# Kernel tuning notes

Measured on AMD Instinct MI355X. Metric: run time of the kernel, lower is better.

The kernel has to match this reference:

```python
import math
import jax, jax.numpy as jnp
import numpy as np

BATCH, L, H, M, K = 16, 4096, 256, 256, 4

def setup_inputs() -> dict:
    key = jax.random.key(0)
    ks = jax.random.split(key, 12)
    inputs = jax.random.normal(ks[0], (BATCH, L, H), jnp.float32)
    b_std = 1.0 / math.sqrt(H)
    c_std = 1.0 / math.sqrt(M)
    B_param = jax.random.uniform(ks[1], (M, H, 2), jnp.float32, -b_std, b_std)
    C_param = jax.random.uniform(ks[2], (H, M, 2), jnp.float32, -c_std, c_std)
    D = jax.random.normal(ks[3], (H,), jnp.float32)
    enc_w = jax.random.normal(ks[4], (H, H), jnp.float32) * (1.0 / math.sqrt(H))
    enc_b = jnp.zeros((H,), jnp.float32)
    conv_w = jax.random.normal(ks[5], (H, 1, K), jnp.float32) * (1.0 / math.sqrt(K))
    conv_b = jnp.zeros((H,), jnp.float32)
    # ring init: r in [0.9,1.0], theta in (0,pi)
    r0 = jnp.sqrt(jax.random.uniform(ks[6], (M,), jnp.float32) * (1.0 - 0.81) + 0.81)
    r0 = jnp.clip(r0, 0.9, 0.999)
    th0 = jax.random.uniform(ks[7], (M,), jnp.float32, 0.05, math.pi - 0.05)
    r_logit_base = jnp.log(r0 / (1.0 - r0))
    th_atanh_base = jnp.arctanh(th0 / math.pi)
    # heads are zero-init in the module; use small random so the selective path is exercised
    r_head_w = jax.random.normal(ks[8], (M, H), jnp.float32) * 0.01
    th_head_w = jax.random.normal(ks[9], (M, H), jnp.float32) * 0.01
    dt_base = jax.random.normal(ks[10], (M,), jnp.float32) * 0.5
    inj_head_w = jax.random.normal(ks[11], (M, H), jnp.float32) * 0.01
    return {"inputs": inputs, "B_param": B_param, "C_param": C_param, "D": D,
            "enc_w": enc_w, "enc_b": enc_b, "conv_w": conv_w, "conv_b": conv_b,
            "r_logit_base": r_logit_base, "th_atanh_base": th_atanh_base,
            "r_head_w": r_head_w, "th_head_w": th_head_w, "dt_base": dt_base,
            "inj_head_w": inj_head_w}

def _forward(inputs, B_param, C_param, D, enc_w, enc_b, conv_w, conv_b,
             r_logit_base, th_atanh_base, r_head_w, th_head_w, dt_base, inj_head_w):
    silu = jax.nn.silu
    # encoder: linear -> SiLU -> depthwise causal conv (left pad K-1) -> SiLU
    feats = silu(inputs @ enc_w.T + enc_b)                      # (B,L,H)
    fc = jnp.transpose(feats, (0, 2, 1))                        # (B,H,L)
    conv = jax.lax.conv_general_dilated(
        fc, conv_w, window_strides=(1,), padding=[(K - 1, 0)],
        dimension_numbers=("NCH", "OIH", "NCH"), feature_group_count=H)
    feats = silu(jnp.transpose(conv + conv_b[None, :, None], (0, 2, 1)))  # (B,L,H)
    # spectral conditioning
    r = jax.nn.sigmoid(r_logit_base + feats @ r_head_w.T)       # (B,L,M)
    theta = math.pi * jnp.tanh(th_atanh_base + feats @ th_head_w.T)
    dt = jax.nn.sigmoid(dt_base)                                # (M,) per_step_dt=False
    dtc = jnp.maximum(dt, 1e-6)
    r2 = jnp.maximum(r * r, 1e-8)
    A = jnp.maximum((r2 - 2.0 * r * jnp.cos(theta) + 1.0) / (dtc * dtc * r2), 0.0)
    G = jnp.maximum((1.0 - r2) / (dtc * r2), 0.0)
    # complex input projection + selective injection gate
    bu = jax.lax.complex(inputs @ B_param[..., 0].T, inputs @ B_param[..., 1].T)  # (B,L,M) c64
    gate = jax.nn.sigmoid(feats @ inj_head_w.T)
    bu = bu * gate
    # time-major for scan
    A_s = jnp.transpose(A, (1, 0, 2))
    G_s = jnp.transpose(G, (1, 0, 2))
    bu_s = jnp.transpose(bu, (1, 0, 2))
    z0 = jnp.zeros((inputs.shape[0], M), jnp.complex64)
    x0 = jnp.zeros((inputs.shape[0], M), jnp.complex64)

    def step(carry, t_in):  # imex1 variant
        z, x = carry
        A_t, G_t, bu_t = t_in
        S = 1.0 + dtc * G_t
        z = (z + dtc * (-A_t * x + bu_t)) / jnp.maximum(S, 1e-6)
        x = x + dtc * z
        return (z, x), x

    _, xs = jax.lax.scan(step, (z0, x0), (A_s, G_s, bu_s))      # (L,B,M) complex64
    proj = (jnp.einsum("lbm,hm->lbh", xs.real, C_param[..., 0])
            - jnp.einsum("lbm,hm->lbh", xs.imag, C_param[..., 1]))
    proj = jnp.transpose(proj, (1, 0, 2))                       # (B,L,H)
    return proj + D * inputs

def reference(inputs, B_param, C_param, D, enc_w, enc_b, conv_w, conv_b,
              r_logit_base, th_atanh_base, r_head_w, th_head_w, dt_base, inj_head_w):
    return _forward(inputs, B_param, C_param, D, enc_w, enc_b, conv_w, conv_b,
                    r_logit_base, th_atanh_base, r_head_w, th_head_w, dt_base, inj_head_w)
```

## Files before the change

### kernel.cpp

```cpp
#include <hip/hip_runtime.h>

#define H_ 256
#define M_ 256
#define L_ 4096
#define B_ 16
#define PI_F 3.14159265358979323846f

typedef unsigned short u16;
typedef __attribute__((ext_vector_type(8))) short short8v;
typedef __attribute__((ext_vector_type(4))) float floatx4;
typedef __attribute__((ext_vector_type(2))) float floatx2;

__device__ __forceinline__ float sigm(float x) { return 1.0f / (1.0f + expf(-x)); }
__device__ __forceinline__ u16 f2bf(float f) {
    unsigned int u = __float_as_uint(f);
    unsigned int r = (u + 0x7fff + ((u >> 16) & 1)) >> 16;
    return (u16)r;
}
__device__ __forceinline__ float bf2f(u16 h) { return __uint_as_float(((unsigned int)h) << 16); }
__device__ __forceinline__ void split2(float x, u16& h, u16& l) {
    h = f2bf(x);
    l = f2bf(x - bf2f(h));
}

__global__ __launch_bounds__(256) void k_prep(const float* __restrict__ Bp,
                                              const float* __restrict__ Cp,
                                              const float* __restrict__ enc_w,
                                              const float* __restrict__ Wr,
                                              const float* __restrict__ Wt,
                                              const float* __restrict__ Wg,
                                              const float* __restrict__ dtb,
                                              u16* __restrict__ EWhi, u16* __restrict__ EWlo,
                                              u16* __restrict__ HWhi, u16* __restrict__ HWlo,
                                              u16* __restrict__ GWhi,
                                              u16* __restrict__ WBh,
                                              u16* __restrict__ Chath,
                                              float* __restrict__ dtc, float* __restrict__ idt,
                                              float* __restrict__ idt2) {
    int tid = blockIdx.x * 256 + threadIdx.x;
    if (tid < M_) {
        float d = fmaxf(sigm(dtb[tid]), 1e-6f);
        dtc[tid] = d;
        idt[tid] = 1.0f / d;
        idt2[tid] = 1.0f / (d * d);
    }
    u16 h, l;
    split2(enc_w[tid], h, l); EWhi[tid] = h; EWlo[tid] = l;
    split2(Wr[tid], h, l);    HWhi[tid] = h; HWlo[tid] = l;
    split2(Wt[tid], h, l);    HWhi[65536 + tid] = h; HWlo[65536 + tid] = l;
    GWhi[tid] = f2bf(Wg[tid]);
    WBh[tid]         = f2bf(Bp[2 * tid + 0]);
    WBh[65536 + tid] = f2bf(Bp[2 * tid + 1]);
    int hh = tid >> 8, m = tid & (M_ - 1);
    Chath[hh * 512 + 2 * m + 0] = f2bf(Cp[2 * tid + 0]);
    Chath[hh * 512 + 2 * m + 1] = f2bf(-Cp[2 * tid + 1]);
}

__global__ __launch_bounds__(256) void k_zero(float* __restrict__ p, int n) {
    int i = blockIdx.x * 256 + threadIdx.x;
    if (i < n) p[i] = 0.0f;
}

template <int NH, int NPROD, int EPI, bool AGLOB>
__global__ __launch_bounds__(256) void k_sgemm(const float* __restrict__ A,
                                               const u16* __restrict__ Whi,
                                               const u16* __restrict__ Wlo,
                                               void* __restrict__ OUTv,
                                               const u16* __restrict__ g16,
                                               const float* __restrict__ p0,
                                               const float* __restrict__ p1,
                                               const float* __restrict__ p2,
                                               const float* __restrict__ p3,
                                               int K, int C, int t0) {
    constexpr int LOR = (NPROD == 3) ? 128 : 1;
    constexpr int NBL = (NPROD == 3) ? NH : 1;
    __shared__ u16 Ah[128][40];
    __shared__ u16 Al[LOR][40];
    __shared__ u16 Bh[NH][128][40];
    __shared__ u16 Bl[NBL][LOR][40];
    const int tid = threadIdx.x;
    const int tpb = C >> 7;
    const int batch = blockIdx.y / tpb;
    const int i0 = (blockIdx.y % tpb) << 7;
    const int colBase = blockIdx.x << 7;
    const int aRow0 = AGLOB ? (batch * L_ + t0 + i0) : (batch * C + i0);
    const int oRow0 = batch * C + i0;
    const int arow = tid >> 1, aseg = (tid & 1) << 4;
    const float* pa = &A[(size_t)(aRow0 + arow) * K + aseg];
    float4 ra0 = *(const float4*)pa, ra1 = *(const float4*)(pa + 4);
    float4 ra2 = *(const float4*)(pa + 8), ra3 = *(const float4*)(pa + 12);
    const int lane = tid & 63, wv = tid >> 6;
    const int wr = wv >> 1, wc = wv & 1;
    const int fr = lane & 15, kg = lane >> 4;
    floatx4 acc[NH][4][4];
#pragma unroll
    for (int h = 0; h < NH; ++h)
#pragma unroll
        for (int i = 0; i < 4; ++i)
#pragma unroll
            for (int j = 0; j < 4; ++j) acc[h][i][j] = (floatx4){0.f, 0.f, 0.f, 0.f};
    const int KT = K >> 5;
    for (int kt = 0; kt < KT; ++kt) {
        short8v rbh[NH][2], rbl[NBL][2];
#pragma unroll
        for (int h = 0; h < NH; ++h) {
            const u16* pb = &Whi[(size_t)h * 65536 + (size_t)(colBase + arow) * K + kt * 32 + aseg];
            rbh[h][0] = *(const short8v*)pb; rbh[h][1] = *(const short8v*)(pb + 8);
            if (NPROD == 3) {
                const u16* pl = &Wlo[(size_t)h * 65536 + (size_t)(colBase + arow) * K + kt * 32 + aseg];
                rbl[h][0] = *(const short8v*)pl; rbl[h][1] = *(const short8v*)(pl + 8);
            }
        }
        __syncthreads();
        {
            u16 hb[16], lb[16];
            float v[16] = {ra0.x, ra0.y, ra0.z, ra0.w, ra1.x, ra1.y, ra1.z, ra1.w,
                           ra2.x, ra2.y, ra2.z, ra2.w, ra3.x, ra3.y, ra3.z, ra3.w};
#pragma unroll
            for (int s = 0; s < 16; ++s) {
                if (NPROD == 3) split2(v[s], hb[s], lb[s]);
                else hb[s] = f2bf(v[s]);
            }
            *(short8v*)&Ah[arow][aseg] = *(short8v*)&hb[0];
            *(short8v*)&Ah[arow][aseg + 8] = *(short8v*)&hb[8];
            if (NPROD == 3) {
                *(short8v*)&Al[arow][aseg] = *(short8v*)&lb[0];
                *(short8v*)&Al[arow][aseg + 8] = *(short8v*)&lb[8];
            }
        }
#pragma unroll
        for (int h = 0; h < NH; ++h) {
            *(short8v*)&Bh[h][arow][aseg] = rbh[h][0];
            *(short8v*)&Bh[h][arow][aseg + 8] = rbh[h][1];
            if (NPROD == 3) {
                *(short8v*)&Bl[h][arow][aseg] = rbl[h][0];
                *(short8v*)&Bl[h][arow][aseg + 8] = rbl[h][1];
            }
        }
        __syncthreads();
        if (kt + 1 < KT) {
            pa += 32;
            ra0 = *(const float4*)pa; ra1 = *(const float4*)(pa + 4);
            ra2 = *(const float4*)(pa + 8); ra3 = *(const float4*)(pa + 12);
        }
        short8v afh[4], afl[4];
#pragma unroll
        for (int i = 0; i < 4; ++i) afh[i] = *(short8v*)&Ah[wr * 64 + i * 16 + fr][kg << 3];
        if (NPROD == 3) {
#pragma unroll
            for (int i = 0; i < 4; ++i) afl[i] = *(short8v*)&Al[wr * 64 + i * 16 + fr][kg << 3];
        }
#pragma unroll
        for (int h = 0; h < NH; ++h) {
            short8v bfh[4], bfl[4];
#pragma unroll
            for (int j = 0; j < 4; ++j) bfh[j] = *(short8v*)&Bh[h][wc * 64 + j * 16 + fr][kg << 3];
            if (h < NBL && NPROD == 3) {
#pragma unroll
                for (int j = 0; j < 4; ++j) bfl[j] = *(short8v*)&Bl[h][wc * 64 + j * 16 + fr][kg << 3];
            }
#pragma unroll
            for (int i = 0; i < 4; ++i)
#pragma unroll
                for (int j = 0; j < 4; ++j) {
                    floatx4 t = acc[h][i][j];
                    if (NPROD == 3) {
                        t = __builtin_amdgcn_mfma_f32_16x16x32_bf16(afl[i], bfh[j], t, 0, 0, 0);
                        t = __builtin_amdgcn_mfma_f32_16x16x32_bf16(afh[i], bfl[j], t, 0, 0, 0);
                    }
                    t = __builtin_amdgcn_mfma_f32_16x16x32_bf16(afh[i], bfh[j], t, 0, 0, 0);
                    acc[h][i][j] = t;
                }
        }
    }
#pragma unroll
    for (int i = 0; i < 4; ++i)
#pragma unroll
        for (int j = 0; j < 4; ++j) {
            int rbase = wr * 64 + i * 16 + (kg << 2);
            int col = colBase + wc * 64 + j * 16 + fr;
#pragma unroll
            for (int r = 0; r < 4; ++r) {
                int orow = oRow0 + rbase + r;
                if (EPI == 1) {
                    float v = acc[0][i][j][r] + p0[col];
                    ((float*)OUTv)[(size_t)orow * 256 + col] = v * sigm(v);
                } else if (EPI == 2) {
                    ((u16*)OUTv)[(size_t)orow * 256 + col] = f2bf(sigm(acc[0][i][j][r]));
                } else if (EPI == 0) {
                    float rr = sigm(p0[col] + acc[0][i][j][r]);
                    float th = PI_F * tanhf(p1[col] + acc[1][i][j][r]);
                    float r2 = fmaxf(rr * rr, 1e-8f);
                    float Av = fmaxf((r2 - 2.0f * rr * cosf(th) + 1.0f) * p3[col] / r2, 0.0f);
                    float Gv = fmaxf((1.0f - r2) * p2[col] / r2, 0.0f);
                    floatx2 o = (floatx2){Av, Gv};
                    __builtin_nontemporal_store(o, (floatx2*)&((float*)OUTv)[((size_t)orow * 256 + col) * 2]);
                } else {
                    float g = bf2f(g16[(size_t)orow * 256 + col]);
#pragma unroll
                    for (int h = 0; h < NH; ++h)
                        __builtin_nontemporal_store(f2bf(acc[h][i][j][r] * g),
                                                    &((u16*)OUTv)[(size_t)orow * 512 + h * 256 + col]);
                }
            }
        }
}

__global__ __launch_bounds__(256) void k_conv(const float* __restrict__ F0,
                                              const float* __restrict__ TAIL,
                                              const float* __restrict__ cw,
                                              const float* __restrict__ cb,
                                              float* __restrict__ F,
                                              int t0, int C) {
    int idx = blockIdx.x * 256 + threadIdx.x;
    int h = idx & (H_ - 1);
    int rl = idx >> 8;
    int b = rl / C;
    int dtl = rl - b * C;
    int t = t0 + dtl;
    float w0 = cw[h * 4 + 0], w1 = cw[h * 4 + 1], w2 = cw[h * 4 + 2], w3 = cw[h * 4 + 3];
    float acc = cb[h];
    acc = fmaf(F0[(size_t)rl * H_ + h], w3, acc);
#pragma unroll
    for (int kk = 1; kk <= 3; ++kk) {
        float w = (kk == 1) ? w2 : (kk == 2) ? w1 : w0;
        if (t - kk >= 0) {
            float src;
            if (dtl - kk >= 0) src = F0[(size_t)(rl - kk) * H_ + h];
            else               src = TAIL[((b * 3 + (3 + dtl - kk)) << 8) + h];
            acc = fmaf(src, w, acc);
        }
    }
    F[(size_t)rl * H_ + h] = acc * sigm(acc);
}

__global__ __launch_bounds__(256) void k_tail(const float* __restrict__ F0,
                                              float* __restrict__ TAIL, int C) {
    int b = blockIdx.x / 3, j = blockIdx.x % 3, h = threadIdx.x;
    TAIL[((b * 3 + j) << 8) + h] = F0[((size_t)(b * C + C - 3 + j) << 8) + h];
}

#define SEG_ 64
__global__ __launch_bounds__(256) void k_scan1(const float* __restrict__ AGf2,
                                               const u16* __restrict__ BUh,
                                               const float* __restrict__ dtc_,
                                               float* __restrict__ SEGM,
                                               float* __restrict__ SEGV,
                                               int C) {
    int m = threadIdx.x;
    int nseg = C >> 6;
    int b = blockIdx.x / nseg;
    int s = blockIdx.x - b * nseg;
    float dt = dtc_[m];
    size_t row0 = (size_t)b * C + s * SEG_;
    float a = 1.f, bb = 0.f, c = 0.f, d = 1.f;
    float vzr = 0.f, vzi = 0.f, vxr = 0.f, vxi = 0.f;
    for (int t = 0; t < SEG_; ++t) {
        size_t row = row0 + t;
        float2 ag = *(const float2*)&AGf2[(row * 256 + m) * 2];
        float br = bf2f(BUh[row * 512 + m]);
        float bi = bf2f(BUh[row * 512 + 256 + m]);
        float S = fmaf(dt, ag.y, 1.0f);
        float e = 1.0f / fmaxf(S, 1e-6f);
        float sa = e;
        float sb = -dt * ag.x * e;
        float sc = dt * e;
        float sd = fmaf(dt, sb, 1.0f);
        float na = fmaf(sa, a, sb * c), nb = fmaf(sa, bb, sb * d);
        float nc = fmaf(sc, a, sd * c), nd = fmaf(sc, bb, sd * d);
        float wz = dt * e;
        float nvzr = fmaf(sa, vzr, fmaf(sb, vxr, wz * br));
        float nvzi = fmaf(sa, vzi, fmaf(sb, vxi, wz * bi));
        float nvxr = fmaf(sc, vzr, fmaf(sd, vxr, dt * wz * br));
        float nvxi = fmaf(sc, vzi, fmaf(sd, vxi, dt * wz * bi));
        a = na; bb = nb; c = nc; d = nd;
        vzr = nvzr; vzi = nvzi; vxr = nvxr; vxi = nvxi;
    }
    size_t o = ((size_t)blockIdx.x * M_ + m) * 4;
    *(float4*)&SEGM[o] = make_float4(a, bb, c, d);
    *(float4*)&SEGV[o] = make_float4(vzr, vzi, vxr, vxi);
}

__global__ __launch_bounds__(256) void k_scan2(const float* __restrict__ SEGM,
                                               const float* __restrict__ SEGV,
                                               float* __restrict__ carry,
                                               float* __restrict__ PRE,
                                               int C) {
    int m = threadIdx.x;
    int b = blockIdx.x;
    int nseg = C >> 6;
    float4 st = *(float4*)&carry[(size_t)(b * M_ + m) * 4];
    for (int s = 0; s < nseg; ++s) {
        size_t o = ((size_t)(b * nseg + s) * M_ + m) * 4;
        *(float4*)&PRE[o] = st;
        float4 Mm = *(const float4*)&SEGM[o];
        float4 Vv = *(const float4*)&SEGV[o];
        float nzr = fmaf(Mm.x, st.x, fmaf(Mm.y, st.z, Vv.x));
        float nzi = fmaf(Mm.x, st.y, fmaf(Mm.y, st.w, Vv.y));
        float nxr = fmaf(Mm.z, st.x, fmaf(Mm.w, st.z, Vv.z));
        float nxi = fmaf(Mm.z, st.y, fmaf(Mm.w, st.w, Vv.w));
        st = make_float4(nzr, nzi, nxr, nxi);
    }
    *(float4*)&carry[(size_t)(b * M_ + m) * 4] = st;
}

__global__ __launch_bounds__(256) void k_scan3p(const float* __restrict__ AGf2,
                                                const u16* __restrict__ BUh,
                                                const float* __restrict__ dtc_,
                                                const float* __restrict__ PRE,
                                                const u16* __restrict__ Chath,
                                                const float* __restrict__ Dv,
                                                const float* __restrict__ X0,
                                                float* __restrict__ OUT,
                                                int t0, int C) {
    __shared__ u16 XT[32][520];
    __shared__ u16 Bs[256][40];
    const int tid = threadIdx.x;
    const int m = tid;
    const int nseg = C >> 6;
    const int b = blockIdx.x / nseg;
    const int s = blockIdx.x - b * nseg;
    const float dt = dtc_[m];
    float4 st = *(const float4*)&PRE[((size_t)blockIdx.x * M_ + m) * 4];
    float zr = st.x, zi = st.y, xr = st.z, xi = st.w;
    const size_t row0 = (size_t)b * C + s * SEG_;
    const int grow0 = b * L_ + t0 + s * SEG_;
    const int lane = tid & 63, wc = tid >> 6;
    const int fr = lane & 15, kg = lane >> 4;
#pragma unroll
    for (int half = 0; half < 2; ++half) {
        for (int t = 0; t < 32; ++t) {
            size_t row = row0 + half * 32 + t;
            floatx2 ag = __builtin_nontemporal_load((const floatx2*)&AGf2[(row * 256 + m) * 2]);
            float br = bf2f(__builtin_nontemporal_load(&BUh[row * 512 + m]));
            float bi = bf2f(__builtin_nontemporal_load(&BUh[row * 512 + 256 + m]));
            float S = fmaf(dt, ag[1], 1.0f);
            float inv = 1.0f / fmaxf(S, 1e-6f);
            zr = fmaf(dt, fmaf(-ag[0], xr, br), zr) * inv;
            zi = fmaf(dt, fmaf(-ag[0], xi, bi), zi) * inv;
            xr = fmaf(dt, zr, xr);
            xi = fmaf(dt, zi, xi);
            unsigned int pk = (unsigned int)f2bf(xr) | ((unsigned int)f2bf(xi) << 16);
            *(unsigned int*)&XT[t][2 * m] = pk;
        }
        __syncthreads();
        floatx4 pacc[2][4];
#pragma unroll
        for (int i = 0; i < 2; ++i)
#pragma unroll
            for (int j = 0; j < 4; ++j) pacc[i][j] = (floatx4){0.f, 0.f, 0.f, 0.f};
        for (int kc = 0; kc < 16; ++kc) {
            const u16* pc = &Chath[(size_t)tid * 512 + kc * 32];
            short8v c0 = *(const short8v*)pc;
            short8v c1 = *(const short8v*)(pc + 8);
            short8v c2 = *(const short8v*)(pc + 16);
            short8v c3 = *(const short8v*)(pc + 24);
            *(short8v*)&Bs[tid][0]  = c0;
            *(short8v*)&Bs[tid][8]  = c1;
            *(short8v*)&Bs[tid][16] = c2;
            *(short8v*)&Bs[tid][24] = c3;
            __syncthreads();
            short8v af[2], bf[4];
#pragma unroll
            for (int i = 0; i < 2; ++i) af[i] = *(short8v*)&XT[i * 16 + fr][kc * 32 + (kg << 3)];
#pragma unroll
            for (int j = 0; j < 4; ++j) bf[j] = *(short8v*)&Bs[wc * 64 + j * 16 + fr][kg << 3];
#pragma unroll
            for (int i = 0; i < 2; ++i)
#pragma unroll
                for (int j = 0; j < 4; ++j)
                    pacc[i][j] = __builtin_amdgcn_mfma_f32_16x16x32_bf16(af[i], bf[j], pacc[i][j], 0, 0, 0);
            __syncthreads();
        }
#pragma unroll
        for (int i = 0; i < 2; ++i)
#pragma unroll
            for (int j = 0; j < 4; ++j) {
                int col = wc * 64 + j * 16 + fr;
#pragma unroll
                for (int r = 0; r < 4; ++r) {
                    int grow = grow0 + half * 32 + i * 16 + (kg << 2) + r;
                    float x0 = __builtin_nontemporal_load(&X0[(size_t)grow * 256 + col]);
                    __builtin_nontemporal_store(fmaf(Dv[col], x0, pacc[i][j][r]),
                                                &OUT[(size_t)grow * 256 + col]);
                }
            }
        __syncthreads();
    }
}

extern "C" void kernel_launch(void* const* d_in, const int* in_sizes, int n_in,
                              void* d_out, int out_size, void* d_ws, size_t ws_size,
                              hipStream_t stream) {
    const float* inputs = (const float*)d_in[0];
    const float* Bp     = (const float*)d_in[1];
    const float* Cp     = (const float*)d_in[2];
    const float* Dv     = (const float*)d_in[3];
    const float* enc_w  = (const float*)d_in[4];
    const float* enc_b  = (const float*)d_in[5];
    const float* conv_w = (const float*)d_in[6];
    const float* conv_b = (const float*)d_in[7];
    const float* rlb    = (const float*)d_in[8];
    const float* tab    = (const float*)d_in[9];
    const float* Wr     = (const float*)d_in[10];
    const float* Wt     = (const float*)d_in[11];
    const float* dtb    = (const float*)d_in[12];
    const float* Wg     = (const float*)d_in[13];

    int C = 4096;
    while (C > 128) {
        size_t need = (size_t)B_ * C * 5632 + (48ull << 20);
        if (need <= ws_size) break;
        C >>= 1;
    }

    char* ws = (char*)d_ws;
    size_t off = 0;
    auto alloc = [&](size_t bytes) -> char* {
        char* p = ws + off;
        off = (off + bytes + 1023) & ~(size_t)1023;
        return p;
    };
    const int rows = B_ * C;
    const int nseg = C >> 6;
    float* F0   = (float*)alloc((size_t)rows * 256 * 4);
    float* F    = (float*)alloc((size_t)rows * 256 * 4);
    float* AGf2 = (float*)alloc((size_t)rows * 512 * 4);
    u16*   GTh  = (u16*)alloc((size_t)rows * 256 * 2);
    u16*   BUh  = (u16*)alloc((size_t)rows * 512 * 2);
    float* SEGM = (float*)alloc((size_t)B_ * nseg * M_ * 16);
    float* SEGV = (float*)alloc((size_t)B_ * nseg * M_ * 16);
    float* PRE  = (float*)alloc((size_t)B_ * nseg * M_ * 16);
    u16* EWhi = (u16*)alloc(65536 * 2);
    u16* EWlo = (u16*)alloc(65536 * 2);
    u16* HWhi = (u16*)alloc(2 * 65536 * 2);
    u16* HWlo = (u16*)alloc(2 * 65536 * 2);
    u16* GWhi = (u16*)alloc(65536 * 2);
    u16* WBh  = (u16*)alloc(2 * 65536 * 2);
    u16* Chath= (u16*)alloc(2 * 65536 * 2);
    float* dtc  = (float*)alloc(1024);
    float* idt  = (float*)alloc(1024);
    float* idt2 = (float*)alloc(1024);
    float* carry= (float*)alloc(B_ * M_ * 16);
    float* TAIL = (float*)alloc(B_ * 3 * 256 * 4);

    const int NC = L_ / C;
    const int tpb = C >> 7;

    k_prep<<<256, 256, 0, stream>>>(Bp, Cp, enc_w, Wr, Wt, Wg, dtb,
                                    EWhi, EWlo, HWhi, HWlo, GWhi, WBh, Chath, dtc, idt, idt2);
    k_zero<<<(B_ * M_ * 4 + 255) / 256, 256, 0, stream>>>(carry, B_ * M_ * 4);

    for (int c = 0; c < NC; ++c) {
        int t0 = c * C;
        k_sgemm<1, 3, 1, true><<<dim3(2, B_ * tpb), 256, 0, stream>>>(
            inputs, EWhi, EWlo, F0, nullptr, enc_b, nullptr, nullptr, nullptr, 256, C, t0);
        k_conv<<<rows, 256, 0, stream>>>(F0, TAIL, conv_w, conv_b, F, t0, C);
        if (NC > 1) k_tail<<<B_ * 3, 256, 0, stream>>>(F0, TAIL, C);
        k_sgemm<2, 3, 0, false><<<dim3(2, B_ * tpb), 256, 0, stream>>>(
            F, HWhi, HWlo, AGf2, nullptr, rlb, tab, idt, idt2, 256, C, t0);
        k_sgemm<1, 1, 2, false><<<dim3(2, B_ * tpb), 256, 0, stream>>>(
            F, GWhi, nullptr, GTh, nullptr, nullptr, nullptr, nullptr, nullptr, 256, C, t0);
        k_sgemm<2, 1, 3, true><<<dim3(2, B_ * tpb), 256, 0, stream>>>(
            inputs, WBh, nullptr, BUh, GTh, nullptr, nullptr, nullptr, nullptr, 256, C, t0);
        k_scan1<<<B_ * nseg, 256, 0, stream>>>(AGf2, BUh, dtc, SEGM, SEGV, C);
        k_scan2<<<B_, 256, 0, stream>>>(SEGM, SEGV, carry, PRE, C);
        k_scan3p<<<B_ * nseg, 256, 0, stream>>>(AGf2, BUh, dtc, PRE, Chath, Dv, inputs,
                                                (float*)d_out, t0, C);
    }
}
```

Baseline: 728.2 us.

## Load weight MFMA fragments directly from global memory, dropping LDS staging

Both the split-bf16 GEMM kernel and the scan projection kernel stop copying weight tiles (Whi/Wlo and Chath) into shared memory. Each wave now reads its MFMA B fragments straight from global memory. This removes the LDS stores and frees LDS for occupancy, and in the scan kernel it also drops two barriers per k-chunk. In exchange, each wave re-fetches the same weight rows from global/L2 with 16-byte strided accesses and loses the register prefetch that overlapped the weight load with compute.

```diff
diff --git a/kernel.cpp b/kernel.cpp
--- a/kernel.cpp
+++ b/kernel.cpp
@@ -73,11 +73,8 @@
                                                const float* __restrict__ p3,
                                                int K, int C, int t0) {
     constexpr int LOR = (NPROD == 3) ? 128 : 1;
-    constexpr int NBL = (NPROD == 3) ? NH : 1;
     __shared__ u16 Ah[128][40];
     __shared__ u16 Al[LOR][40];
-    __shared__ u16 Bh[NH][128][40];
-    __shared__ u16 Bl[NBL][LOR][40];
     const int tid = threadIdx.x;
     const int tpb = C >> 7;
     const int batch = blockIdx.y / tpb;
@@ -101,16 +98,6 @@
             for (int j = 0; j < 4; ++j) acc[h][i][j] = (floatx4){0.f, 0.f, 0.f, 0.f};
     const int KT = K >> 5;
     for (int kt = 0; kt < KT; ++kt) {
-        short8v rbh[NH][2], rbl[NBL][2];
-#pragma unroll
-        for (int h = 0; h < NH; ++h) {
-            const u16* pb = &Whi[(size_t)h * 65536 + (size_t)(colBase + arow) * K + kt * 32 + aseg];
-            rbh[h][0] = *(const short8v*)pb; rbh[h][1] = *(const short8v*)(pb + 8);
-            if (NPROD == 3) {
-                const u16* pl = &Wlo[(size_t)h * 65536 + (size_t)(colBase + arow) * K + kt * 32 + aseg];
-                rbl[h][0] = *(const short8v*)pl; rbl[h][1] = *(const short8v*)(pl + 8);
-            }
-        }
         __syncthreads();
         {
             u16 hb[16], lb[16];
@@ -128,15 +115,6 @@
                 *(short8v*)&Al[arow][aseg + 8] = *(short8v*)&lb[8];
             }
         }
-#pragma unroll
-        for (int h = 0; h < NH; ++h) {
-            *(short8v*)&Bh[h][arow][aseg] = rbh[h][0];
-            *(short8v*)&Bh[h][arow][aseg + 8] = rbh[h][1];
-            if (NPROD == 3) {
-                *(short8v*)&Bl[h][arow][aseg] = rbl[h][0];
-                *(short8v*)&Bl[h][arow][aseg + 8] = rbl[h][1];
-            }
-        }
         __syncthreads();
         if (kt + 1 < KT) {
             pa += 32;
@@ -154,10 +132,14 @@
         for (int h = 0; h < NH; ++h) {
             short8v bfh[4], bfl[4];
 #pragma unroll
-            for (int j = 0; j < 4; ++j) bfh[j] = *(short8v*)&Bh[h][wc * 64 + j * 16 + fr][kg << 3];
-            if (h < NBL && NPROD == 3) {
-#pragma unroll
-                for (int j = 0; j < 4; ++j) bfl[j] = *(short8v*)&Bl[h][wc * 64 + j * 16 + fr][kg << 3];
+            for (int j = 0; j < 4; ++j)
+                bfh[j] = *(const short8v*)&Whi[(size_t)h * 65536 +
+                          (size_t)(colBase + wc * 64 + j * 16 + fr) * K + kt * 32 + (kg << 3)];
+            if (NPROD == 3) {
+#pragma unroll
+                for (int j = 0; j < 4; ++j)
+                    bfl[j] = *(const short8v*)&Wlo[(size_t)h * 65536 +
+                              (size_t)(colBase + wc * 64 + j * 16 + fr) * K + kt * 32 + (kg << 3)];
             }
 #pragma unroll
             for (int i = 0; i < 4; ++i)
@@ -314,7 +296,6 @@
                                                 float* __restrict__ OUT,
                                                 int t0, int C) {
     __shared__ u16 XT[32][520];
-    __shared__ u16 Bs[256][40];
     const int tid = threadIdx.x;
     const int m = tid;
     const int nseg = C >> 6;
@@ -350,27 +331,17 @@
 #pragma unroll
             for (int j = 0; j < 4; ++j) pacc[i][j] = (floatx4){0.f, 0.f, 0.f, 0.f};
         for (int kc = 0; kc < 16; ++kc) {
-            const u16* pc = &Chath[(size_t)tid * 512 + kc * 32];
-            short8v c0 = *(const short8v*)pc;
-            short8v c1 = *(const short8v*)(pc + 8);
-            short8v c2 = *(const short8v*)(pc + 16);
-            short8v c3 = *(const short8v*)(pc + 24);
-            *(short8v*)&Bs[tid][0]  = c0;
-            *(short8v*)&Bs[tid][8]  = c1;
-            *(short8v*)&Bs[tid][16] = c2;
-            *(short8v*)&Bs[tid][24] = c3;
-            __syncthreads();
             short8v af[2], bf[4];
 #pragma unroll
             for (int i = 0; i < 2; ++i) af[i] = *(short8v*)&XT[i * 16 + fr][kc * 32 + (kg << 3)];
 #pragma unroll
-            for (int j = 0; j < 4; ++j) bf[j] = *(short8v*)&Bs[wc * 64 + j * 16 + fr][kg << 3];
+            for (int j = 0; j < 4; ++j)
+                bf[j] = *(const short8v*)&Chath[(size_t)(wc * 64 + j * 16 + fr) * 512 + kc * 32 + (kg << 3)];
 #pragma unroll
             for (int i = 0; i < 2; ++i)
 #pragma unroll
                 for (int j = 0; j < 4; ++j)
                     pacc[i][j] = __builtin_amdgcn_mfma_f32_16x16x32_bf16(af[i], bf[j], pacc[i][j], 0, 0, 0);
-            __syncthreads();
         }
 #pragma unroll
         for (int i = 0; i < 2; ++i)
```

Measured after the change: 840.5 us. +15.4%, slower.

## Pre-split GEMM inputs to bf16 planes and stage tiles via global_load_lds

Applied to the files above, without the earlier changes.

Converts the fp32 inputs and the conv output into bf16 hi/lo planes ahead of time, so the GEMM kernels no longer split fp32 to bf16 inside their main loop. The GEMM is rewritten to copy each tile straight from global memory into LDS with global_load_lds into unpadded planes, which removes the register round trip and the convert work. Costs include an extra conversion pass over the whole input, a larger workspace, possible LDS bank conflicts from the unpadded 32-wide rows, and a second barrier per k-step with no prefetch overlap.

```diff
diff --git a/kernel.cpp b/kernel.cpp
--- a/kernel.cpp
+++ b/kernel.cpp
@@ -21,6 +21,11 @@
 __device__ __forceinline__ void split2(float x, u16& h, u16& l) {
     h = f2bf(x);
     l = f2bf(x - bf2f(h));
+}
+__device__ __forceinline__ void gload16(const u16* gsrc, u16* ldst) {
+    typedef __attribute__((address_space(1))) const unsigned int GU;
+    typedef __attribute__((address_space(3))) unsigned int LU;
+    __builtin_amdgcn_global_load_lds((GU*)gsrc, (LU*)ldst, 16, 0, 0);
 }
 
 __global__ __launch_bounds__(256) void k_prep(const float* __restrict__ Bp,
@@ -61,8 +66,22 @@
     if (i < n) p[i] = 0.0f;
 }
 
-template <int NH, int NPROD, int EPI, bool AGLOB>
-__global__ __launch_bounds__(256) void k_sgemm(const float* __restrict__ A,
+__global__ __launch_bounds__(256) void k_tobf(const float* __restrict__ X,
+                                              u16* __restrict__ Xhi, u16* __restrict__ Xlo) {
+    size_t i = ((size_t)blockIdx.x * 256 + threadIdx.x) * 8;
+    float4 a = *(const float4*)&X[i];
+    float4 b = *(const float4*)&X[i + 4];
+    float v[8] = {a.x, a.y, a.z, a.w, b.x, b.y, b.z, b.w};
+    u16 hb[8], lb[8];
+#pragma unroll
+    for (int s = 0; s < 8; ++s) split2(v[s], hb[s], lb[s]);
+    *(short8v*)&Xhi[i] = *(short8v*)hb;
+    *(short8v*)&Xlo[i] = *(short8v*)lb;
+}
+
+template <int NH, int NSPLIT, int EPI, bool AGLOB>
+__global__ __launch_bounds__(256) void k_bgemm(const u16* __restrict__ Ahi,
+                                               const u16* __restrict__ Alo,
                                                const u16* __restrict__ Whi,
                                                const u16* __restrict__ Wlo,
                                                void* __restrict__ OUTv,
@@ -71,13 +90,10 @@
                                                const float* __restrict__ p1,
                                                const float* __restrict__ p2,
                                                const float* __restrict__ p3,
-                                               int K, int C, int t0) {
-    constexpr int LOR = (NPROD == 3) ? 128 : 1;
-    constexpr int NBL = (NPROD == 3) ? NH : 1;
-    __shared__ u16 Ah[128][40];
-    __shared__ u16 Al[LOR][40];
-    __shared__ u16 Bh[NH][128][40];
-    __shared__ u16 Bl[NBL][LOR][40];
+                                               int C, int t0) {
+    constexpr int NA = (NSPLIT > 0) ? 2 : 1;
+    constexpr int NPLANES = NA + NH + NSPLIT;
+    __shared__ u16 LDS[NPLANES * 4096];
     const int tid = threadIdx.x;
     const int tpb = C >> 7;
     const int batch = blockIdx.y / tpb;
@@ -85,13 +101,20 @@
     const int colBase = blockIdx.x << 7;
     const int aRow0 = AGLOB ? (batch * L_ + t0 + i0) : (batch * C + i0);
     const int oRow0 = batch * C + i0;
-    const int arow = tid >> 1, aseg = (tid & 1) << 4;
-    const float* pa = &A[(size_t)(aRow0 + arow) * K + aseg];
-    float4 ra0 = *(const float4*)pa, ra1 = *(const float4*)(pa + 4);
-    float4 ra2 = *(const float4*)(pa + 8), ra3 = *(const float4*)(pa + 12);
+    const u16* gp[NPLANES];
+    {
+        int idx = 0;
+        gp[idx++] = Ahi + (size_t)aRow0 * 256;
+        if (NA == 2) gp[idx++] = Alo + (size_t)aRow0 * 256;
+#pragma unroll
+        for (int h = 0; h < NH; ++h) gp[idx++] = Whi + (size_t)h * 65536 + (size_t)colBase * 256;
+#pragma unroll
+        for (int h = 0; h < NSPLIT; ++h) gp[idx++] = Wlo + (size_t)h * 65536 + (size_t)colBase * 256;
+    }
     const int lane = tid & 63, wv = tid >> 6;
     const int wr = wv >> 1, wc = wv & 1;
     const int fr = lane & 15, kg = lane >> 4;
+    const int wbase = (tid & 192) * 8;
     floatx4 acc[NH][4][4];
 #pragma unroll
     for (int h = 0; h < NH; ++h)
@@ -99,72 +122,50 @@
         for (int i = 0; i < 4; ++i)
 #pragma unroll
             for (int j = 0; j < 4; ++j) acc[h][i][j] = (floatx4){0.f, 0.f, 0.f, 0.f};
-    const int KT = K >> 5;
-    for (int kt = 0; kt < KT; ++kt) {
-        short8v rbh[NH][2], rbl[NBL][2];
-#pragma unroll
-        for (int h = 0; h < NH; ++h) {
-            const u16* pb = &Whi[(size_t)h * 65536 + (size_t)(colBase + arow) * K + kt * 32 + aseg];
-            rbh[h][0] = *(const short8v*)pb; rbh[h][1] = *(const short8v*)(pb + 8);
-            if (NPROD == 3) {
-                const u16* pl = &Wlo[(size_t)h * 65536 + (size_t)(colBase + arow) * K + kt * 32 + aseg];
-                rbl[h][0] = *(const short8v*)pl; rbl[h][1] = *(const short8v*)(pl + 8);
-            }
-        }
+    for (int kt = 0; kt < 8; ++kt) {
+#pragma unroll
+        for (int p = 0; p < NPLANES; ++p)
+#pragma unroll
+            for (int q = 0; q < 2; ++q) {
+                int slot = q * 256 + tid;
+                const u16* src = gp[p] + (size_t)(slot >> 2) * 256 + kt * 32 + (slot & 3) * 8;
+                gload16(src, &LDS[p * 4096 + q * 2048 + wbase]);
+            }
         __syncthreads();
-        {
-            u16 hb[16], lb[16];
-            float v[16] = {ra0.x, ra0.y, ra0.z, ra0.w, ra1.x, ra1.y, ra1.z, ra1.w,
-                           ra2.x, ra2.y, ra2.z, ra2.w, ra3.x, ra3.y, ra3.z, ra3.w};
-#pragma unroll
-            for (int s = 0; s < 16; ++s) {
-                if (NPROD == 3) split2(v[s], hb[s], lb[s]);
-                else hb[s] = f2bf(v[s]);
-            }
-            *(short8v*)&Ah[arow][aseg] = *(short8v*)&hb[0];
-            *(short8v*)&Ah[arow][aseg + 8] = *(short8v*)&hb[8];
-            if (NPROD == 3) {
-                *(short8v*)&Al[arow][aseg] = *(short8v*)&lb[0];
-                *(short8v*)&Al[arow][aseg + 8] = *(short8v*)&lb[8];
-            }
-        }
-#pragma unroll
-        for (int h = 0; h < NH; ++h) {
-            *(short8v*)&Bh[h][arow][aseg] = rbh[h][0];
-            *(short8v*)&Bh[h][arow][aseg + 8] = rbh[h][1];
-            if (NPROD == 3) {
-                *(short8v*)&Bl[h][arow][aseg] = rbl[h][0];
-                *(short8v*)&Bl[h][arow][aseg + 8] = rbl[h][1];
-            }
-        }
-        __syncthreads();
-        if (kt + 1 < KT) {
-            pa += 32;
-            ra0 = *(const float4*)pa; ra1 = *(const float4*)(pa + 4);
-            ra2 = *(const float4*)(pa + 8); ra3 = *(const float4*)(pa + 12);
-        }
         short8v afh[4], afl[4];
 #pragma unroll
-        for (int i = 0; i < 4; ++i) afh[i] = *(short8v*)&Ah[wr * 64 + i * 16 + fr][kg << 3];
-        if (NPROD == 3) {
-#pragma unroll
-            for (int i = 0; i < 4; ++i) afl[i] = *(short8v*)&Al[wr * 64 + i * 16 + fr][kg << 3];
+        for (int i = 0; i < 4; ++i) {
+            int row = wr * 64 + i * 16 + fr;
+            afh[i] = *(short8v*)&LDS[row * 32 + kg * 8];
+        }
+        if (NA == 2) {
+#pragma unroll
+            for (int i = 0; i < 4; ++i) {
+                int row = wr * 64 + i * 16 + fr;
+                afl[i] = *(short8v*)&LDS[4096 + row * 32 + kg * 8];
+            }
         }
 #pragma unroll
         for (int h = 0; h < NH; ++h) {
             short8v bfh[4], bfl[4];
 #pragma unroll
-            for (int j = 0; j < 4; ++j) bfh[j] = *(short8v*)&Bh[h][wc * 64 + j * 16 + fr][kg << 3];
-            if (h < NBL && NPROD == 3) {
-#pragma unroll
-                for (int j = 0; j < 4; ++j) bfl[j] = *(short8v*)&Bl[h][wc * 64 + j * 16 + fr][kg << 3];
+            for (int j = 0; j < 4; ++j) {
+                int row = wc * 64 + j * 16 + fr;
+                bfh[j] = *(short8v*)&LDS[(NA + h) * 4096 + row * 32 + kg * 8];
+            }
+            if (h < NSPLIT) {
+#pragma unroll
+                for (int j = 0; j < 4; ++j) {
+                    int row = wc * 64 + j * 16 + fr;
+                    bfl[j] = *(short8v*)&LDS[(NA + NH + h) * 4096 + row * 32 + kg * 8];
+                }
             }
 #pragma unroll
             for (int i = 0; i < 4; ++i)
 #pragma unroll
                 for (int j = 0; j < 4; ++j) {
                     floatx4 t = acc[h][i][j];
-                    if (NPROD == 3) {
+                    if (h < NSPLIT) {
                         t = __builtin_amdgcn_mfma_f32_16x16x32_bf16(afl[i], bfh[j], t, 0, 0, 0);
                         t = __builtin_amdgcn_mfma_f32_16x16x32_bf16(afh[i], bfl[j], t, 0, 0, 0);
                     }
@@ -172,6 +173,7 @@
                     acc[h][i][j] = t;
                 }
         }
+        __syncthreads();
     }
 #pragma unroll
     for (int i = 0; i < 4; ++i)
@@ -210,7 +212,8 @@
                                               const float* __restrict__ TAIL,
                                               const float* __restrict__ cw,
                                               const float* __restrict__ cb,
-                                              float* __restrict__ F,
+                                              u16* __restrict__ Fhi,
+                                              u16* __restrict__ Flo,
                                               int t0, int C) {
     int idx = blockIdx.x * 256 + threadIdx.x;
     int h = idx & (H_ - 1);
@@ -231,7 +234,11 @@
             acc = fmaf(src, w, acc);
         }
     }
-    F[(size_t)rl * H_ + h] = acc * sigm(acc);
+    float y = acc * sigm(acc);
+    u16 hh, ll;
+    split2(y, hh, ll);
+    Fhi[(size_t)rl * H_ + h] = hh;
+    Flo[(size_t)rl * H_ + h] = ll;
 }
 
 __global__ __launch_bounds__(256) void k_tail(const float* __restrict__ F0,
@@ -409,7 +416,7 @@
 
     int C = 4096;
     while (C > 128) {
-        size_t need = (size_t)B_ * C * 5632 + (48ull << 20);
+        size_t need = (size_t)B_ * C * 7168 + (64ull << 20);
         if (need <= ws_size) break;
         C >>= 1;
     }
@@ -424,7 +431,10 @@
     const int rows = B_ * C;
     const int nseg = C >> 6;
     float* F0   = (float*)alloc((size_t)rows * 256 * 4);
-    float* F    = (float*)alloc((size_t)rows * 256 * 4);
+    u16*   Fhi  = (u16*)alloc((size_t)rows * 256 * 2);
+    u16*   Flo  = (u16*)alloc((size_t)rows * 256 * 2);
+    u16*   Xhi  = (u16*)alloc((size_t)B_ * L_ * 256 * 2);
+    u16*   Xlo  = (u16*)alloc((size_t)B_ * L_ * 256 * 2);
     float* AGf2 = (float*)alloc((size_t)rows * 512 * 4);
     u16*   GTh  = (u16*)alloc((size_t)rows * 256 * 2);
     u16*   BUh  = (u16*)alloc((size_t)rows * 512 * 2);
@@ -450,19 +460,20 @@
     k_prep<<<256, 256, 0, stream>>>(Bp, Cp, enc_w, Wr, Wt, Wg, dtb,
                                     EWhi, EWlo, HWhi, HWlo, GWhi, WBh, Chath, dtc, idt, idt2);
     k_zero<<<(B_ * M_ * 4 + 255) / 256, 256, 0, stream>>>(carry, B_ * M_ * 4);
+    k_tobf<<<(B_ * L_ * 256) / (256 * 8), 256, 0, stream>>>(inputs, Xhi, Xlo);
 
     for (int c = 0; c < NC; ++c) {
         int t0 = c * C;
-        k_sgemm<1, 3, 1, true><<<dim3(2, B_ * tpb), 256, 0, stream>>>(
-            inputs, EWhi, EWlo, F0, nullptr, enc_b, nullptr, nullptr, nullptr, 256, C, t0);
-        k_conv<<<rows, 256, 0, stream>>>(F0, TAIL, conv_w, conv_b, F, t0, C);
+        k_bgemm<1, 1, 1, true><<<dim3(2, B_ * tpb), 256, 0, stream>>>(
+            Xhi, Xlo, EWhi, EWlo, F0, nullptr, enc_b, nullptr, nullptr, nullptr, C, t0);
+        k_conv<<<rows, 256, 0, stream>>>(F0, TAIL, conv_w, conv_b, Fhi, Flo, t0, C);
         if (NC > 1) k_tail<<<B_ * 3, 256, 0, stream>>>(F0, TAIL, C);
-        k_sgemm<2, 3, 0, false><<<dim3(2, B_ * tpb), 256, 0, stream>>>(
-            F, HWhi, HWlo, AGf2, nullptr, rlb, tab, idt, idt2, 256, C, t0);
-        k_sgemm<1, 1, 2, false><<<dim3(2, B_ * tpb), 256, 0, stream>>>(
-            F, GWhi, nullptr, GTh, nullptr, nullptr, nullptr, nullptr, nullptr, 256, C, t0);
-        k_sgemm<2, 1, 3, true><<<dim3(2, B_ * tpb), 256, 0, stream>>>(
-            inputs, WBh, nullptr, BUh, GTh, nullptr, nullptr, nullptr, nullptr, 256, C, t0);
+        k_bgemm<2, 2, 0, false><<<dim3(2, B_ * tpb), 256, 0, stream>>>(
+            Fhi, Flo, HWhi, HWlo, AGf2, nullptr, rlb, tab, idt, idt2, C, t0);
+        k_bgemm<1, 0, 2, false><<<dim3(2, B_ * tpb), 256, 0, stream>>>(
+            Fhi, nullptr, GWhi, nullptr, GTh, nullptr, nullptr, nullptr, nullptr, nullptr, C, t0);
+        k_bgemm<2, 0, 3, true><<<dim3(2, B_ * tpb), 256, 0, stream>>>(
+            Xhi, nullptr, WBh, nullptr, BUh, GTh, nullptr, nullptr, nullptr, nullptr, C, t0);
         k_scan1<<<B_ * nseg, 256, 0, stream>>>(AGf2, BUh, dtc, SEGM, SEGV, C);
         k_scan2<<<B_, 256, 0, stream>>>(SEGM, SEGV, carry, PRE, C);
         k_scan3p<<<B_ * nseg, 256, 0, stream>>>(AGf2, BUh, dtc, PRE, Chath, Dv, inputs,
```

Result: slower. 970.5 us (+33.3%).
